# Optimization experiments

Measured on AMD Instinct MI355X. Metric: run time of the kernel, lower is better.

## Reference

```python
import jax, jax.numpy as jnp
import numpy as np

D_MODEL = 1024
NUM_EXPERTS = 64
TOP_K = 2
TEMPERATURE = 1.0


def setup_inputs() -> dict:
    key = jax.random.key(0)
    k1, k2, k3, k4 = jax.random.split(key, 4)
    mh_output = jax.random.normal(k1, (8, 4096, D_MODEL), dtype=jnp.float32)
    noise = jax.random.normal(k2, (8, 4096, NUM_EXPERTS), dtype=jnp.float32)  # randn_like sample, externalized
    # nn.Linear weights: shape [out, in], init normal(0, 0.02); biases zero
    W_route = jax.random.normal(k3, (NUM_EXPERTS, D_MODEL), dtype=jnp.float32) * 0.02
    b_route = jnp.zeros((NUM_EXPERTS,), dtype=jnp.float32)
    W_noise = jax.random.normal(k4, (NUM_EXPERTS, D_MODEL), dtype=jnp.float32) * 0.02
    b_noise = jnp.zeros((NUM_EXPERTS,), dtype=jnp.float32)
    return {"mh_output": mh_output, "noise": noise, "W_route": W_route,
            "b_route": b_route, "W_noise": W_noise, "b_noise": b_noise}


def reference(mh_output, noise, W_route, b_route, W_noise, b_noise):
    # logits = topkroute_linear(mh_output); noise_logits = noise_linear(mh_output)
    logits = jnp.einsum('bsd,ed->bse', mh_output, W_route) + b_route
    noise_logits = jnp.einsum('bsd,ed->bse', mh_output, W_noise) + b_noise
    # noisy logits = logits + temperature * randn * softplus(noise_logits)
    noisy = logits + TEMPERATURE * noise * jax.nn.softplus(noise_logits)
    # top-k, scatter into -inf, softmax  ==  softmax over top-k values scattered into zeros
    top_vals, indices = jax.lax.top_k(noisy, TOP_K)          # [b, s, k]
    probs_k = jax.nn.softmax(top_vals, axis=-1)              # softmax(-inf elsewhere) -> 0 elsewhere
    one_hot = jax.nn.one_hot(indices, NUM_EXPERTS, dtype=noisy.dtype)  # [b, s, k, E]
    router_output = jnp.sum(one_hot * probs_k[..., None], axis=-2)     # [b, s, E]
    return router_output, indices
```

## Files before the change

### kernel.cpp

```cpp
#include <hip/hip_runtime.h>
#include <hip/hip_bf16.h>
#include <math.h>


#define T_TOKENS 32768
#define D_MODEL  1024
#define NE       64
#define NCOL     128
#define M_TILE   64
#define NCHUNK   32
#define RING_D   4
#define CS_LD    68
#define OUT_IDX_BASE ((size_t)T_TOKENS * NE)
#define W_ELEMS  (NCOL * D_MODEL)

typedef short  bf16x8  __attribute__((ext_vector_type(8)));
typedef float  floatx4 __attribute__((ext_vector_type(4)));
typedef const __attribute__((address_space(1))) unsigned int gu32;
typedef __attribute__((address_space(3))) unsigned int lu32;

__device__ __forceinline__ float softplus_f(float x) {
    return fmaxf(x, 0.f) + log1pf(expf(-fabsf(x)));
}

__device__ __forceinline__ void cvt8(const float4 a, const float4 b,
                                     int4* hi, int4* lo) {
    float v[8] = {a.x, a.y, a.z, a.w, b.x, b.y, b.z, b.w};
    int hw[4], lw[4];
    #pragma unroll
    for (int p = 0; p < 4; ++p) {
        float2 f2 = make_float2(v[2 * p], v[2 * p + 1]);
        __hip_bfloat162 h2 = __float22bfloat162_rn(f2);
        int u; __builtin_memcpy(&u, &h2, 4);
        float h0 = __uint_as_float(((unsigned)u) << 16);
        float h1 = __uint_as_float(((unsigned)u) & 0xFFFF0000u);
        float2 l2 = make_float2(v[2 * p] - h0, v[2 * p + 1] - h1);
        __hip_bfloat162 L2 = __float22bfloat162_rn(l2);
        int ul; __builtin_memcpy(&ul, &L2, 4);
        hw[p] = u; lw[p] = ul;
    }
    *hi = make_int4(hw[0], hw[1], hw[2], hw[3]);
    *lo = make_int4(lw[0], lw[1], lw[2], lw[3]);
}

__device__ __forceinline__ void cvt8r(const float4 a, const float4 b,
                                      bf16x8* hi, bf16x8* lo) {
    int4 h, l;
    cvt8(a, b, &h, &l);
    __builtin_memcpy(hi, &h, 16);
    __builtin_memcpy(lo, &l, 16);
}

__global__ __launch_bounds__(256) void prepack_w(
    const float* __restrict__ Wr, const float* __restrict__ Wn,
    short* __restrict__ Bh, short* __restrict__ Bl)
{
    int g   = blockIdx.x * 256 + threadIdx.x;
    int n   = g & 15;
    int kg  = (g >> 4) & 127;
    int t2  = g >> 11;
    int col = t2 * 16 + n;
    const float* src = (col < NE ? Wr + (size_t)col * D_MODEL
                                 : Wn + (size_t)(col - NE) * D_MODEL) + kg * 8;
    float4 a = *(const float4*)src;
    float4 b = *(const float4*)(src + 4);
    int4 hi, lo;
    cvt8(a, b, &hi, &lo);
    *(int4*)(Bh + (size_t)g * 8) = hi;
    *(int4*)(Bl + (size_t)g * 8) = lo;
}

__global__ __launch_bounds__(256, 2) void router_mfma(
    const float* __restrict__ A,
    const float* __restrict__ noise,
    const float* __restrict__ br,
    const float* __restrict__ bn,
    const short* __restrict__ Bh,
    const short* __restrict__ Bl,
    float* __restrict__ out)
{
    __shared__ __align__(16) float ringA[RING_D * M_TILE * 32];
    __shared__ float Cs[M_TILE * CS_LD];
    __shared__ float s_p1[M_TILE], s_p2[M_TILE];
    __shared__ int   s_e1[M_TILE], s_e2[M_TILE];

    const int tid  = threadIdx.x;
    const int lane = tid & 63;
    const int wid  = tid >> 6;
    const int n16  = lane & 15;
    const int quad = lane >> 4;
    const int m0   = blockIdx.x * M_TILE;

    const int rlo = lane >> 3;
    const int c4  = (lane & 7) * 4;
    const int j0  = 2 * wid;
    const float* srcA0 = A + (size_t)(m0 + j0 * 8 + rlo) * D_MODEL + c4;
    const float* srcA1 = A + (size_t)(m0 + j0 * 8 + 8 + rlo) * D_MODEL + c4;

    const short* pBhR = Bh + ((size_t)(wid * 128 + quad) * 16 + n16) * 8;
    const short* pBlR = Bl + ((size_t)(wid * 128 + quad) * 16 + n16) * 8;
    const short* pBhN = Bh + ((size_t)((4 + wid) * 128 + quad) * 16 + n16) * 8;
    const short* pBlN = Bl + ((size_t)((4 + wid) * 128 + quad) * 16 + n16) * 8;

#define DMA_CHUNK(KC_) do {                                                   \
        const int b_ = (KC_) & (RING_D - 1);                                  \
        __builtin_amdgcn_global_load_lds(                                     \
            (gu32*)(srcA0 + (KC_) * 32),                                      \
            (lu32*)(ringA + b_ * (M_TILE * 32) + j0 * 256), 16, 0, 0);        \
        __builtin_amdgcn_global_load_lds(                                     \
            (gu32*)(srcA1 + (KC_) * 32),                                      \
            (lu32*)(ringA + b_ * (M_TILE * 32) + (j0 + 1) * 256), 16, 0, 0);  \
    } while (0)

    floatx4 acc[4][2];
    #pragma unroll
    for (int i = 0; i < 4; ++i) { acc[i][0] = (floatx4)0.f; acc[i][1] = (floatx4)0.f; }

    DMA_CHUNK(0);
    DMA_CHUNK(1);
    DMA_CHUNK(2);
    bf16x8 b0hR = *(const bf16x8*)(pBhR);
    bf16x8 b0lR = *(const bf16x8*)(pBlR);
    bf16x8 b0hN = *(const bf16x8*)(pBhN);
    bf16x8 b0lN = *(const bf16x8*)(pBlN);
    bf16x8 b1hR = *(const bf16x8*)(pBhR + 512);
    bf16x8 b1lR = *(const bf16x8*)(pBlR + 512);
    bf16x8 b1hN = *(const bf16x8*)(pBhN + 512);
    bf16x8 b1lN = *(const bf16x8*)(pBlN + 512);

    #pragma unroll 1
    for (int kc = 0; kc < NCHUNK; ++kc) {
        const int buf = kc & (RING_D - 1);

        bf16x8 b2hR, b2lR, b2hN, b2lN;
        if (kc + 2 < NCHUNK) {
            const int o = (kc + 2) * 512;
            b2hR = *(const bf16x8*)(pBhR + o);
            b2lR = *(const bf16x8*)(pBlR + o);
            b2hN = *(const bf16x8*)(pBhN + o);
            b2lN = *(const bf16x8*)(pBlN + o);
        }
        __builtin_amdgcn_sched_barrier(0);

        if (kc == 0)            asm volatile("s_waitcnt vmcnt(8)"  ::: "memory");
        else if (kc == 1)       asm volatile("s_waitcnt vmcnt(10)" ::: "memory");
        else if (kc < NCHUNK-2) asm volatile("s_waitcnt vmcnt(12)" ::: "memory");
        else if (kc == NCHUNK-2)asm volatile("s_waitcnt vmcnt(4)"  ::: "memory");
        else                    asm volatile("s_waitcnt vmcnt(0)"  ::: "memory");
        __builtin_amdgcn_s_barrier();
        __builtin_amdgcn_sched_barrier(0);

        if (kc + 3 < NCHUNK) DMA_CHUNK(kc + 3);

        float4 fa[4], fb[4];
        #pragma unroll
        for (int mf = 0; mf < 4; ++mf) {
            const float* p = &ringA[buf * (M_TILE * 32) + (mf * 16 + n16) * 32 + quad * 8];
            fa[mf] = *(const float4*)(p);
            fb[mf] = *(const float4*)(p + 4);
        }

        #pragma unroll
        for (int mf = 0; mf < 4; ++mf) {
            bf16x8 ah, al;
            cvt8r(fa[mf], fb[mf], &ah, &al);
            acc[mf][0] = __builtin_amdgcn_mfma_f32_16x16x32_bf16(ah, b0hR, acc[mf][0], 0, 0, 0);
            acc[mf][0] = __builtin_amdgcn_mfma_f32_16x16x32_bf16(ah, b0lR, acc[mf][0], 0, 0, 0);
            acc[mf][0] = __builtin_amdgcn_mfma_f32_16x16x32_bf16(al, b0hR, acc[mf][0], 0, 0, 0);
            acc[mf][1] = __builtin_amdgcn_mfma_f32_16x16x32_bf16(ah, b0hN, acc[mf][1], 0, 0, 0);
            acc[mf][1] = __builtin_amdgcn_mfma_f32_16x16x32_bf16(ah, b0lN, acc[mf][1], 0, 0, 0);
            acc[mf][1] = __builtin_amdgcn_mfma_f32_16x16x32_bf16(al, b0hN, acc[mf][1], 0, 0, 0);
        }

        b0hR = b1hR; b0lR = b1lR; b0hN = b1hN; b0lN = b1lN;
        b1hR = b2hR; b1lR = b2lR; b1hN = b2hN; b1lN = b2lN;
    }
#undef DMA_CHUNK

    {
        int e = wid * 16 + n16;
        float brv = br[e], bnv = bn[e];
        #pragma unroll
        for (int mf = 0; mf < 4; ++mf)
            #pragma unroll
            for (int rr = 0; rr < 4; ++rr) {
                int t = mf * 16 + quad * 4 + rr;
                float nz    = noise[(size_t)(m0 + t) * NE + e];
                float route = acc[mf][0][rr] + brv;
                float nl    = acc[mf][1][rr] + bnv;
                Cs[t * CS_LD + e] = fmaf(nz, softplus_f(nl), route);
            }
    }
    __syncthreads();

    if (tid < M_TILE) {
        const int t = tid;
        float v1 = -INFINITY, v2 = -INFINITY;
        int e1 = 0, e2 = 0;
        #pragma unroll
        for (int e4 = 0; e4 < 16; ++e4) {
            float4 q = *(const float4*)&Cs[t * CS_LD + e4 * 4];
            float qa[4] = {q.x, q.y, q.z, q.w};
            #pragma unroll
            for (int c = 0; c < 4; ++c) {
                float v = qa[c];
                int e = e4 * 4 + c;
                if (v > v1) { v2 = v1; e2 = e1; v1 = v; e1 = e; }
                else if (v > v2) { v2 = v; e2 = e; }
            }
        }
        float ex = expf(v2 - v1);
        float denom = 1.f + ex;
        s_p1[t] = 1.f / denom;
        s_p2[t] = ex / denom;
        s_e1[t] = e1;
        s_e2[t] = e2;
        float2 iv = make_float2((float)e1, (float)e2);
        *(float2*)(out + OUT_IDX_BASE + (size_t)(m0 + t) * 2) = iv;
    }
    __syncthreads();

    #pragma unroll
    for (int i = 0; i < 4; ++i) {
        int gi = i * 256 + tid;
        int t  = gi >> 4;
        int e0 = (gi & 15) * 4;
        float p1 = s_p1[t], p2 = s_p2[t];
        int   e1 = s_e1[t], e2 = s_e2[t];
        float4 v;
        v.x = (e0 + 0 == e1) ? p1 : ((e0 + 0 == e2) ? p2 : 0.f);
        v.y = (e0 + 1 == e1) ? p1 : ((e0 + 1 == e2) ? p2 : 0.f);
        v.z = (e0 + 2 == e1) ? p1 : ((e0 + 2 == e2) ? p2 : 0.f);
        v.w = (e0 + 3 == e1) ? p1 : ((e0 + 3 == e2) ? p2 : 0.f);
        *(float4*)(out + (size_t)(m0 + t) * NE + e0) = v;
    }
}

extern "C" void kernel_launch(void* const* d_in, const int* in_sizes, int n_in,
                              void* d_out, int out_size, void* d_ws, size_t ws_size,
                              hipStream_t stream) {
    const float* A     = (const float*)d_in[0];
    const float* noise = (const float*)d_in[1];
    const float* Wr    = (const float*)d_in[2];
    const float* br    = (const float*)d_in[3];
    const float* Wn    = (const float*)d_in[4];
    const float* bn    = (const float*)d_in[5];
    float* out = (float*)d_out;

    short* Bh = (short*)d_ws;
    short* Bl = Bh + W_ELEMS;

    prepack_w<<<dim3(W_ELEMS / 8 / 256), dim3(256), 0, stream>>>(Wr, Wn, Bh, Bl);
    router_mfma<<<dim3(T_TOKENS / M_TILE), dim3(256), 0, stream>>>(A, noise, br, bn, Bh, Bl, out);
}
```

Measured before the change: 234.3 us.

## Shrink token tile to 16 and pre-convert whole A panel to bf16 in LDS

The token tile drops from 64 to 16 rows per block. Each thread loads its slice of the full 16x1024 activation panel into registers, splits it into bf16 hi/lo parts once, and writes them into padded LDS. The MFMA loop then runs fully unrolled with no barriers or async DMA ring. This removes the per-chunk barrier/waitcnt pipeline and the repeated conversion work, and launches 4x more blocks for better load balance. In exchange, the packed weights are re-read by 4x more blocks, each block does less work relative to its setup cost, and there is no overlap between the A load and compute inside a block.

```diff
diff --git a/kernel.cpp b/kernel.cpp
--- a/kernel.cpp
+++ b/kernel.cpp
@@ -7,17 +7,15 @@
 #define D_MODEL  1024
 #define NE       64
 #define NCOL     128
-#define M_TILE   64
+#define M_TILE   16
 #define NCHUNK   32
-#define RING_D   4
+#define SUBS     136
 #define CS_LD    68
 #define OUT_IDX_BASE ((size_t)T_TOKENS * NE)
 #define W_ELEMS  (NCOL * D_MODEL)
 
 typedef short  bf16x8  __attribute__((ext_vector_type(8)));
 typedef float  floatx4 __attribute__((ext_vector_type(4)));
-typedef const __attribute__((address_space(1))) unsigned int gu32;
-typedef __attribute__((address_space(3))) unsigned int lu32;
 
 __device__ __forceinline__ float softplus_f(float x) {
     return fmaxf(x, 0.f) + log1pf(expf(-fabsf(x)));
@@ -43,12 +41,23 @@
     *lo = make_int4(lw[0], lw[1], lw[2], lw[3]);
 }
 
-__device__ __forceinline__ void cvt8r(const float4 a, const float4 b,
-                                      bf16x8* hi, bf16x8* lo) {
-    int4 h, l;
-    cvt8(a, b, &h, &l);
-    __builtin_memcpy(hi, &h, 16);
-    __builtin_memcpy(lo, &l, 16);
+__device__ __forceinline__ void cvt4(const float4 a, int2* hi, int2* lo) {
+    float v[4] = {a.x, a.y, a.z, a.w};
+    int hw[2], lw[2];
+    #pragma unroll
+    for (int p = 0; p < 2; ++p) {
+        float2 f2 = make_float2(v[2 * p], v[2 * p + 1]);
+        __hip_bfloat162 h2 = __float22bfloat162_rn(f2);
+        int u; __builtin_memcpy(&u, &h2, 4);
+        float h0 = __uint_as_float(((unsigned)u) << 16);
+        float h1 = __uint_as_float(((unsigned)u) & 0xFFFF0000u);
+        float2 l2 = make_float2(v[2 * p] - h0, v[2 * p + 1] - h1);
+        __hip_bfloat162 L2 = __float22bfloat162_rn(l2);
+        int ul; __builtin_memcpy(&ul, &L2, 4);
+        hw[p] = u; lw[p] = ul;
+    }
+    *hi = make_int2(hw[0], hw[1]);
+    *lo = make_int2(lw[0], lw[1]);
 }
 
 __global__ __launch_bounds__(256) void prepack_w(
@@ -79,46 +88,32 @@
     const short* __restrict__ Bl,
     float* __restrict__ out)
 {
-    __shared__ __align__(16) float ringA[RING_D * M_TILE * 32];
-    __shared__ float Cs[M_TILE * CS_LD];
+    __shared__ __align__(16) short Ah[NCHUNK * 4 * SUBS];
+    __shared__ __align__(16) short Al[NCHUNK * 4 * SUBS];
+    __shared__ float Ns[M_TILE * CS_LD];
     __shared__ float s_p1[M_TILE], s_p2[M_TILE];
     __shared__ int   s_e1[M_TILE], s_e2[M_TILE];
+    float* Cs = reinterpret_cast<float*>(&Ah[0]);
 
     const int tid  = threadIdx.x;
     const int lane = tid & 63;
     const int wid  = tid >> 6;
     const int n16  = lane & 15;
     const int quad = lane >> 4;
-    const int m0   = blockIdx.x * M_TILE;
-
-    const int rlo = lane >> 3;
-    const int c4  = (lane & 7) * 4;
-    const int j0  = 2 * wid;
-    const float* srcA0 = A + (size_t)(m0 + j0 * 8 + rlo) * D_MODEL + c4;
-    const float* srcA1 = A + (size_t)(m0 + j0 * 8 + 8 + rlo) * D_MODEL + c4;
+    const size_t blk = blockIdx.x;
+    const int m0   = (int)blk * M_TILE;
+
+    const float* panel = A + blk * (size_t)(M_TILE * D_MODEL);
+    float4 f[16];
+    #pragma unroll
+    for (int i = 0; i < 16; ++i)
+        f[i] = *(const float4*)(panel + i * D_MODEL + tid * 4);
+    float4 nzf = *(const float4*)(noise + blk * (size_t)(M_TILE * NE) + tid * 4);
 
     const short* pBhR = Bh + ((size_t)(wid * 128 + quad) * 16 + n16) * 8;
     const short* pBlR = Bl + ((size_t)(wid * 128 + quad) * 16 + n16) * 8;
     const short* pBhN = Bh + ((size_t)((4 + wid) * 128 + quad) * 16 + n16) * 8;
     const short* pBlN = Bl + ((size_t)((4 + wid) * 128 + quad) * 16 + n16) * 8;
-
-#define DMA_CHUNK(KC_) do {                                                   \
-        const int b_ = (KC_) & (RING_D - 1);                                  \
-        __builtin_amdgcn_global_load_lds(                                     \
-            (gu32*)(srcA0 + (KC_) * 32),                                      \
-            (lu32*)(ringA + b_ * (M_TILE * 32) + j0 * 256), 16, 0, 0);        \
-        __builtin_amdgcn_global_load_lds(                                     \
-            (gu32*)(srcA1 + (KC_) * 32),                                      \
-            (lu32*)(ringA + b_ * (M_TILE * 32) + (j0 + 1) * 256), 16, 0, 0);  \
-    } while (0)
-
-    floatx4 acc[4][2];
-    #pragma unroll
-    for (int i = 0; i < 4; ++i) { acc[i][0] = (floatx4)0.f; acc[i][1] = (floatx4)0.f; }
-
-    DMA_CHUNK(0);
-    DMA_CHUNK(1);
-    DMA_CHUNK(2);
     bf16x8 b0hR = *(const bf16x8*)(pBhR);
     bf16x8 b0lR = *(const bf16x8*)(pBlR);
     bf16x8 b0hN = *(const bf16x8*)(pBhN);
@@ -128,68 +123,56 @@
     bf16x8 b1hN = *(const bf16x8*)(pBhN + 512);
     bf16x8 b1lN = *(const bf16x8*)(pBlN + 512);
 
-    #pragma unroll 1
-    for (int kc = 0; kc < NCHUNK; ++kc) {
-        const int buf = kc & (RING_D - 1);
-
+    {
+        const int sb    = (tid >> 3) * 4 + ((tid >> 1) & 3);
+        const int dbase = sb * SUBS + (tid & 1) * 4;
+        #pragma unroll
+        for (int i = 0; i < 16; ++i) {
+            int2 hi, lo;
+            cvt4(f[i], &hi, &lo);
+            *(int2*)&Ah[dbase + i * 8] = hi;
+            *(int2*)&Al[dbase + i * 8] = lo;
+        }
+        *(float4*)&Ns[(tid >> 4) * CS_LD + (tid & 15) * 4] = nzf;
+    }
+    __syncthreads();
+
+    floatx4 acc0 = (floatx4)0.f, acc1 = (floatx4)0.f;
+    const int aOff = quad * SUBS + n16 * 8;
+    #pragma unroll
+    for (int c = 0; c < NCHUNK; ++c) {
         bf16x8 b2hR, b2lR, b2hN, b2lN;
-        if (kc + 2 < NCHUNK) {
-            const int o = (kc + 2) * 512;
+        if (c + 2 < NCHUNK) {
+            const int o = (c + 2) * 512;
             b2hR = *(const bf16x8*)(pBhR + o);
             b2lR = *(const bf16x8*)(pBlR + o);
             b2hN = *(const bf16x8*)(pBhN + o);
             b2lN = *(const bf16x8*)(pBlN + o);
         }
-        __builtin_amdgcn_sched_barrier(0);
-
-        if (kc == 0)            asm volatile("s_waitcnt vmcnt(8)"  ::: "memory");
-        else if (kc == 1)       asm volatile("s_waitcnt vmcnt(10)" ::: "memory");
-        else if (kc < NCHUNK-2) asm volatile("s_waitcnt vmcnt(12)" ::: "memory");
-        else if (kc == NCHUNK-2)asm volatile("s_waitcnt vmcnt(4)"  ::: "memory");
-        else                    asm volatile("s_waitcnt vmcnt(0)"  ::: "memory");
-        __builtin_amdgcn_s_barrier();
-        __builtin_amdgcn_sched_barrier(0);
-
-        if (kc + 3 < NCHUNK) DMA_CHUNK(kc + 3);
-
-        float4 fa[4], fb[4];
-        #pragma unroll
-        for (int mf = 0; mf < 4; ++mf) {
-            const float* p = &ringA[buf * (M_TILE * 32) + (mf * 16 + n16) * 32 + quad * 8];
-            fa[mf] = *(const float4*)(p);
-            fb[mf] = *(const float4*)(p + 4);
-        }
-
-        #pragma unroll
-        for (int mf = 0; mf < 4; ++mf) {
-            bf16x8 ah, al;
-            cvt8r(fa[mf], fb[mf], &ah, &al);
-            acc[mf][0] = __builtin_amdgcn_mfma_f32_16x16x32_bf16(ah, b0hR, acc[mf][0], 0, 0, 0);
-            acc[mf][0] = __builtin_amdgcn_mfma_f32_16x16x32_bf16(ah, b0lR, acc[mf][0], 0, 0, 0);
-            acc[mf][0] = __builtin_amdgcn_mfma_f32_16x16x32_bf16(al, b0hR, acc[mf][0], 0, 0, 0);
-            acc[mf][1] = __builtin_amdgcn_mfma_f32_16x16x32_bf16(ah, b0hN, acc[mf][1], 0, 0, 0);
-            acc[mf][1] = __builtin_amdgcn_mfma_f32_16x16x32_bf16(ah, b0lN, acc[mf][1], 0, 0, 0);
-            acc[mf][1] = __builtin_amdgcn_mfma_f32_16x16x32_bf16(al, b0hN, acc[mf][1], 0, 0, 0);
-        }
-
+        bf16x8 ah = *(const bf16x8*)&Ah[c * 4 * SUBS + aOff];
+        bf16x8 al = *(const bf16x8*)&Al[c * 4 * SUBS + aOff];
+        acc0 = __builtin_amdgcn_mfma_f32_16x16x32_bf16(ah, b0hR, acc0, 0, 0, 0);
+        acc0 = __builtin_amdgcn_mfma_f32_16x16x32_bf16(ah, b0lR, acc0, 0, 0, 0);
+        acc0 = __builtin_amdgcn_mfma_f32_16x16x32_bf16(al, b0hR, acc0, 0, 0, 0);
+        acc1 = __builtin_amdgcn_mfma_f32_16x16x32_bf16(ah, b0hN, acc1, 0, 0, 0);
+        acc1 = __builtin_amdgcn_mfma_f32_16x16x32_bf16(ah, b0lN, acc1, 0, 0, 0);
+        acc1 = __builtin_amdgcn_mfma_f32_16x16x32_bf16(al, b0hN, acc1, 0, 0, 0);
         b0hR = b1hR; b0lR = b1lR; b0hN = b1hN; b0lN = b1lN;
         b1hR = b2hR; b1lR = b2lR; b1hN = b2hN; b1lN = b2lN;
     }
-#undef DMA_CHUNK
+    __syncthreads();
 
     {
-        int e = wid * 16 + n16;
+        const int e = wid * 16 + n16;
         float brv = br[e], bnv = bn[e];
         #pragma unroll
-        for (int mf = 0; mf < 4; ++mf)
-            #pragma unroll
-            for (int rr = 0; rr < 4; ++rr) {
-                int t = mf * 16 + quad * 4 + rr;
-                float nz    = noise[(size_t)(m0 + t) * NE + e];
-                float route = acc[mf][0][rr] + brv;
-                float nl    = acc[mf][1][rr] + bnv;
-                Cs[t * CS_LD + e] = fmaf(nz, softplus_f(nl), route);
-            }
+        for (int rr = 0; rr < 4; ++rr) {
+            int t = quad * 4 + rr;
+            float nz    = Ns[t * CS_LD + e];
+            float route = acc0[rr] + brv;
+            float nl    = acc1[rr] + bnv;
+            Cs[t * CS_LD + e] = fmaf(nz, softplus_f(nl), route);
+        }
     }
     __syncthreads();
 
@@ -220,11 +203,9 @@
     }
     __syncthreads();
 
-    #pragma unroll
-    for (int i = 0; i < 4; ++i) {
-        int gi = i * 256 + tid;
-        int t  = gi >> 4;
-        int e0 = (gi & 15) * 4;
+    {
+        int t  = tid >> 4;
+        int e0 = (tid & 15) * 4;
         float p1 = s_p1[t], p2 = s_p2[t];
         int   e1 = s_e1[t], e2 = s_e2[t];
         float4 v;
```

Result: slower. 256.2 us (+9.3%).
